# Optimization experiments

Hardware: AMD Instinct MI355X
Metric: run time of the kernel (lower is better)

Reference implementation:

```python
import jax, jax.numpy as jnp
import numpy as np

N_ATOMS = 200_000
AVG_NEIGHBORS = 64
N_PAIRS = N_ATOMS * AVG_NEIGHBORS
BOX = 60.0  # Angstrom, so cutoff=10 masks most random pairs (realistic neighbor-list sparsity)


def setup_inputs() -> dict:
    key = jax.random.key(0)
    kR, ki, kj = jax.random.split(key, 3)
    R = jax.random.uniform(kR, (N_ATOMS, 3), dtype=jnp.float32) * BOX
    idx_i = jax.random.randint(ki, (N_PAIRS,), 0, N_ATOMS, dtype=jnp.int32)
    idx_j = jax.random.randint(kj, (N_PAIRS,), 0, N_ATOMS, dtype=jnp.int32)
    # learned scalar parameters from __init__
    epsilon = jnp.float32(0.238)
    sigma = jnp.float32(3.4)
    cutoff = jnp.float32(10.0)
    return {"R": R, "epsilon": epsilon, "sigma": sigma, "cutoff": cutoff,
            "idx_i": idx_i, "idx_j": idx_j}


def reference(R, epsilon, sigma, cutoff, idx_i, idx_j):
    """LJ 12-6 pairwise potential over a neighbor list.

    Returns (energy [N] per-atom, forces [N,3]).
    Each (i,j) pair appears in both directions in the pair list, hence the 0.5
    factor on per-atom energy; forces accumulate per direction (action-reaction
    handled by the symmetric pair list).
    """
    n_atoms = R.shape[0]
    rij = R[idx_i] - R[idx_j]                     # [P,3] gather
    r2 = jnp.sum(rij * rij, axis=-1)              # [P]
    mask = (r2 < cutoff * cutoff) & (r2 > 1e-10)  # inside cutoff, exclude coincident
    r2s = jnp.where(mask, r2, 1.0)                # safe divide
    sr2 = (sigma * sigma) / r2s
    sr6 = sr2 * sr2 * sr2
    sr12 = sr6 * sr6
    e_pair = jnp.where(mask, 4.0 * epsilon * (sr12 - sr6), 0.0)          # [P]
    f_mag = jnp.where(mask, 24.0 * epsilon * (2.0 * sr12 - sr6) / r2s, 0.0)
    f_pair = f_mag[:, None] * rij                 # [P,3]
    energy = 0.5 * jax.ops.segment_sum(e_pair, idx_i, num_segments=n_atoms)   # [N]
    forces = jax.ops.segment_sum(f_pair, idx_i, num_segments=n_atoms)         # [N,3]
    return energy, forces
```

## Files before the change

### kernel.cpp

```cpp
#include <hip/hip_runtime.h>


typedef int   v4i __attribute__((ext_vector_type(4)));
typedef float v4f __attribute__((ext_vector_type(4)));

#define GRP    8
#define WGT    1024
#define NWG_F  256

__global__ void __launch_bounds__(256) pad_R_kernel(
    const float* __restrict__ R, v4f* __restrict__ Rp, int n_atoms)
{
    int a = blockIdx.x * blockDim.x + threadIdx.x;
    if (a < n_atoms) {
        v4f v;
        v.x = R[3 * a + 0];
        v.y = R[3 * a + 1];
        v.z = R[3 * a + 2];
        v.w = 0.0f;
        Rp[a] = v;
    }
}

__global__ void __launch_bounds__(256) cell_kernel(
    const float* __restrict__ R, const float* __restrict__ cut_p,
    unsigned* __restrict__ packed, int n_atoms)
{
    int t = blockIdx.x * blockDim.x + threadIdx.x;
    int n_thr = (n_atoms + 15) >> 4;
    if (t >= n_thr) return;
    const float inv_cut = 1.0f / cut_p[0];
    int a0 = t << 4;
    unsigned w[3] = {0u, 0u, 0u};
#pragma unroll
    for (int k = 0; k < 16; ++k) {
        int a = a0 + k;
        unsigned c = 0u;
        if (a < n_atoms) {
            int cx = min(7, max(0, (int)(R[3 * a + 0] * inv_cut)));
            int cy = min(7, max(0, (int)(R[3 * a + 1] * inv_cut)));
            c = (unsigned)(cx | (cy << 3));
        }
        int bit = 6 * k, word = bit >> 5, off = bit & 31;
        w[word] |= c << off;
        if (off > 26) w[word + 1] |= c >> (32 - off);
    }
    packed[3 * t + 0] = w[0];
    packed[3 * t + 1] = w[1];
    packed[3 * t + 2] = w[2];
}

__device__ __forceinline__ unsigned cell6(const unsigned char* c8, unsigned a) {
    unsigned bit = a * 6u;
    unsigned by  = bit >> 3;
    unsigned v   = (unsigned)c8[by] | ((unsigned)c8[by + 1] << 8);
    return (v >> (bit & 7u)) & 63u;
}

__device__ __forceinline__ void lj_body(
    v4f A, v4f B, float eps, float s2, float cut2, int gi,
    float* __restrict__ energy, float* __restrict__ forces)
{
    const float dx = A.x - B.x, dy = A.y - B.y, dz = A.z - B.z;
    const float r2 = dx * dx + dy * dy + dz * dz;
    if (r2 < cut2 && r2 > 1e-10f) {
        const float inv  = 1.0f / r2;
        const float sr2  = s2 * inv;
        const float sr6  = sr2 * sr2 * sr2;
        const float sr12 = sr6 * sr6;
        const float e    = 2.0f * eps * (sr12 - sr6);
        const float f    = 24.0f * eps * (2.0f * sr12 - sr6) * inv;
        atomicAdd(&energy[gi], e);
        atomicAdd(&forces[3 * gi + 0], f * dx);
        atomicAdd(&forces[3 * gi + 1], f * dy);
        atomicAdd(&forces[3 * gi + 2], f * dz);
    }
}

__global__ void __launch_bounds__(WGT) lj_fused_kernel(
    const v4f* __restrict__ Rp,
    const unsigned* __restrict__ packed,
    const int* __restrict__ idx_i,
    const int* __restrict__ idx_j,
    const float* __restrict__ eps_p,
    const float* __restrict__ sig_p,
    const float* __restrict__ cut_p,
    float* __restrict__ energy,
    float* __restrict__ forces,
    int n_pairs, int pk_words, int chunk)
{
    extern __shared__ unsigned lds[];
    for (int w = threadIdx.x; w < pk_words; w += WGT)
        lds[w] = packed[w];
    __syncthreads();
    const unsigned char* c8 = (const unsigned char*)lds;

    const float eps  = eps_p[0];
    const float sig  = sig_p[0];
    const float cut  = cut_p[0];
    const float s2   = sig * sig;
    const float cut2 = cut * cut;

    const int cs = blockIdx.x * chunk;
    const int ce = min(cs + chunk, n_pairs);

    for (int p = cs + threadIdx.x * GRP; p < ce; p += WGT * GRP) {
        int is8[GRP], js8[GRP];
        if (p + GRP <= n_pairs) {
            v4i a0 = __builtin_nontemporal_load((const v4i*)idx_i + (p >> 2));
            v4i a1 = __builtin_nontemporal_load((const v4i*)idx_i + (p >> 2) + 1);
            v4i b0 = __builtin_nontemporal_load((const v4i*)idx_j + (p >> 2));
            v4i b1 = __builtin_nontemporal_load((const v4i*)idx_j + (p >> 2) + 1);
            is8[0] = a0.x; is8[1] = a0.y; is8[2] = a0.z; is8[3] = a0.w;
            is8[4] = a1.x; is8[5] = a1.y; is8[6] = a1.z; is8[7] = a1.w;
            js8[0] = b0.x; js8[1] = b0.y; js8[2] = b0.z; js8[3] = b0.w;
            js8[4] = b1.x; js8[5] = b1.y; js8[6] = b1.z; js8[7] = b1.w;
        } else {
#pragma unroll
            for (int k = 0; k < GRP; ++k) {
                bool v = (p + k < n_pairs);
                is8[k] = v ? idx_i[p + k] : 0;
                js8[k] = v ? idx_j[p + k] : 0;
            }
        }

        unsigned m = 0u;
#pragma unroll
        for (int k = 0; k < GRP; ++k) {
            unsigned ci = cell6(c8, (unsigned)is8[k]);
            unsigned cj = cell6(c8, (unsigned)js8[k]);
            int ddx = (int)(ci & 7u) - (int)(cj & 7u);
            int ddy = (int)(ci >> 3) - (int)(cj >> 3);
            bool ok = ((unsigned)(ddx + 1) <= 2u) & ((unsigned)(ddy + 1) <= 2u);
            if (ok) m |= (1u << k);
        }

        v4f Ri[GRP], Rj[GRP];
#pragma unroll
        for (int k = 0; k < GRP; ++k)
            if (m & (1u << k)) { Ri[k] = Rp[is8[k]]; Rj[k] = Rp[js8[k]]; }

#pragma unroll
        for (int k = 0; k < GRP; ++k)
            if (m & (1u << k))
                lj_body(Ri[k], Rj[k], eps, s2, cut2, is8[k], energy, forces);
    }
}

#define PPT 8
__global__ void __launch_bounds__(256) lj_pairs_fb_kernel(
    const v4f* __restrict__ Rp,
    const v4i* __restrict__ idx_i4, const v4i* __restrict__ idx_j4,
    const float* __restrict__ eps_p, const float* __restrict__ sig_p,
    const float* __restrict__ cut_p,
    float* __restrict__ energy, float* __restrict__ forces, int n_oct)
{
    int t = blockIdx.x * blockDim.x + threadIdx.x;
    if (t >= n_oct) return;
    const float eps  = eps_p[0];
    const float sig  = sig_p[0];
    const float cut  = cut_p[0];
    const float s2   = sig * sig;
    const float cut2 = cut * cut;
    v4i ii0 = __builtin_nontemporal_load(idx_i4 + 2 * t);
    v4i ii1 = __builtin_nontemporal_load(idx_i4 + 2 * t + 1);
    v4i jj0 = __builtin_nontemporal_load(idx_j4 + 2 * t);
    v4i jj1 = __builtin_nontemporal_load(idx_j4 + 2 * t + 1);
    int is[PPT] = { ii0.x, ii0.y, ii0.z, ii0.w, ii1.x, ii1.y, ii1.z, ii1.w };
    int js[PPT] = { jj0.x, jj0.y, jj0.z, jj0.w, jj1.x, jj1.y, jj1.z, jj1.w };
    v4f Ri[PPT], Rj[PPT];
#pragma unroll
    for (int k = 0; k < PPT; ++k) Ri[k] = Rp[is[k]];
#pragma unroll
    for (int k = 0; k < PPT; ++k) Rj[k] = Rp[js[k]];
#pragma unroll
    for (int k = 0; k < PPT; ++k)
        lj_body(Ri[k], Rj[k], eps, s2, cut2, is[k], energy, forces);
}

__global__ void lj_pairs_fb_tail_kernel(
    const v4f* __restrict__ Rp,
    const int* __restrict__ idx_i, const int* __restrict__ idx_j,
    const float* __restrict__ eps_p, const float* __restrict__ sig_p,
    const float* __restrict__ cut_p,
    float* __restrict__ energy, float* __restrict__ forces,
    int start, int n_pairs)
{
    int p = start + blockIdx.x * blockDim.x + threadIdx.x;
    if (p >= n_pairs) return;
    const float eps = eps_p[0];
    const float sig = sig_p[0];
    const float cut = cut_p[0];
    lj_body(Rp[idx_i[p]], Rp[idx_j[p]], eps, sig * sig, cut * cut,
            idx_i[p], energy, forces);
}

extern "C" void kernel_launch(void* const* d_in, const int* in_sizes, int n_in,
                              void* d_out, int out_size, void* d_ws, size_t ws_size,
                              hipStream_t stream) {
    const float* R     = (const float*)d_in[0];
    const float* eps_p = (const float*)d_in[1];
    const float* sig_p = (const float*)d_in[2];
    const float* cut_p = (const float*)d_in[3];
    const int*   idx_i = (const int*)d_in[4];
    const int*   idx_j = (const int*)d_in[5];

    const int n_atoms = in_sizes[0] / 3;
    const int n_pairs = in_sizes[4];

    float* energy = (float*)d_out;
    float* forces = (float*)d_out + n_atoms;

    (void)hipMemsetAsync(d_out, 0, (size_t)out_size * sizeof(float), stream);

    char* ws = (char*)d_ws;
    const size_t rp_b     = (((size_t)n_atoms * 16) + 255) & ~(size_t)255;
    const int    n_thr    = (n_atoms + 15) >> 4;
    const int    pk_words = 3 * n_thr + 1;
    const size_t pk_b     = (((size_t)pk_words * 4) + 255) & ~(size_t)255;
    const size_t lds_b    = (((size_t)pk_words * 4) + 15) & ~(size_t)15;

    const bool have_rp    = ws_size >= rp_b;
    const bool use_filter = have_rp && (ws_size >= rp_b + pk_b)
                            && (lds_b <= 160000);

    v4f*      Rp     = (v4f*)ws;
    unsigned* packed = (unsigned*)(ws + rp_b);

    if (have_rp) {
        int blocks = (n_atoms + 255) / 256;
        pad_R_kernel<<<blocks, 256, 0, stream>>>(R, Rp, n_atoms);
    }

    if (use_filter) {
        int cblocks = (n_thr + 255) / 256;
        cell_kernel<<<cblocks, 256, 0, stream>>>(R, cut_p, packed, n_atoms);

        (void)hipFuncSetAttribute((const void*)lj_fused_kernel,
                                  hipFuncAttributeMaxDynamicSharedMemorySize,
                                  (int)lds_b);

        int chunk = (((n_pairs + NWG_F - 1) / NWG_F) + GRP - 1) & ~(GRP - 1);
        lj_fused_kernel<<<NWG_F, WGT, lds_b, stream>>>(
            Rp, packed, idx_i, idx_j, eps_p, sig_p, cut_p,
            energy, forces, n_pairs, pk_words, chunk);
    } else {
        const int n_oct = n_pairs / PPT;
        const int start = n_oct * PPT;
        if (n_oct > 0) {
            int blocks = (n_oct + 255) / 256;
            lj_pairs_fb_kernel<<<blocks, 256, 0, stream>>>(
                Rp, (const v4i*)idx_i, (const v4i*)idx_j,
                eps_p, sig_p, cut_p, energy, forces, n_oct);
        }
        if (start < n_pairs) {
            lj_pairs_fb_tail_kernel<<<1, 64, 0, stream>>>(
                Rp, idx_i, idx_j, eps_p, sig_p, cut_p,
                energy, forces, start, n_pairs);
        }
    }
}
```

Baseline: 192.4 us.

## Fuse prep kernels, use word-aligned cell packing, software-pipeline index loads

```diff
diff --git a/kernel.cpp b/kernel.cpp
--- a/kernel.cpp
+++ b/kernel.cpp
@@ -7,6 +7,33 @@
 #define GRP    8
 #define WGT    1024
 #define NWG_F  256
+
+__global__ void __launch_bounds__(256) prep_kernel(
+    const float* __restrict__ R, const float* __restrict__ cut_p,
+    v4f* __restrict__ Rp, unsigned* __restrict__ packed, int n_atoms)
+{
+    int t = blockIdx.x * blockDim.x + threadIdx.x;
+    int n_grp = (n_atoms + 4) / 5;
+    if (t >= n_grp) return;
+    const float inv_cut = 1.0f / cut_p[0];
+    int a0 = t * 5;
+    unsigned w = 0u;
+#pragma unroll
+    for (int k = 0; k < 5; ++k) {
+        int a = a0 + k;
+        if (a < n_atoms) {
+            float x = R[3 * a + 0];
+            float y = R[3 * a + 1];
+            float z = R[3 * a + 2];
+            v4f v; v.x = x; v.y = y; v.z = z; v.w = 0.0f;
+            Rp[a] = v;
+            int cx = min(7, max(0, (int)(x * inv_cut)));
+            int cy = min(7, max(0, (int)(y * inv_cut)));
+            w |= (unsigned)(cx | (cy << 3)) << (6 * k);
+        }
+    }
+    packed[t] = w;
+}
 
 __global__ void __launch_bounds__(256) pad_R_kernel(
     const float* __restrict__ R, v4f* __restrict__ Rp, int n_atoms)
@@ -22,39 +49,51 @@
     }
 }
 
-__global__ void __launch_bounds__(256) cell_kernel(
-    const float* __restrict__ R, const float* __restrict__ cut_p,
-    unsigned* __restrict__ packed, int n_atoms)
-{
-    int t = blockIdx.x * blockDim.x + threadIdx.x;
-    int n_thr = (n_atoms + 15) >> 4;
-    if (t >= n_thr) return;
-    const float inv_cut = 1.0f / cut_p[0];
-    int a0 = t << 4;
-    unsigned w[3] = {0u, 0u, 0u};
-#pragma unroll
-    for (int k = 0; k < 16; ++k) {
-        int a = a0 + k;
-        unsigned c = 0u;
-        if (a < n_atoms) {
-            int cx = min(7, max(0, (int)(R[3 * a + 0] * inv_cut)));
-            int cy = min(7, max(0, (int)(R[3 * a + 1] * inv_cut)));
-            c = (unsigned)(cx | (cy << 3));
-        }
-        int bit = 6 * k, word = bit >> 5, off = bit & 31;
-        w[word] |= c << off;
-        if (off > 26) w[word + 1] |= c >> (32 - off);
-    }
-    packed[3 * t + 0] = w[0];
-    packed[3 * t + 1] = w[1];
-    packed[3 * t + 2] = w[2];
-}
-
-__device__ __forceinline__ unsigned cell6(const unsigned char* c8, unsigned a) {
-    unsigned bit = a * 6u;
-    unsigned by  = bit >> 3;
-    unsigned v   = (unsigned)c8[by] | ((unsigned)c8[by + 1] << 8);
-    return (v >> (bit & 7u)) & 63u;
+__device__ __forceinline__ unsigned cell6w(const unsigned* __restrict__ lds32,
+                                           unsigned a) {
+    unsigned q = __umulhi(a, 0xCCCCCCCDu) >> 2;
+    unsigned r = a - q * 5u;
+    return (lds32[q] >> (r * 6u)) & 63u;
+}
+
+__device__ __forceinline__ void load_grp(
+    const int* __restrict__ idx_i, const int* __restrict__ idx_j,
+    int p, int n_pairs, int* __restrict__ is8, int* __restrict__ js8)
+{
+    if (p + GRP <= n_pairs) {
+        v4i a0 = __builtin_nontemporal_load((const v4i*)idx_i + (p >> 2));
+        v4i a1 = __builtin_nontemporal_load((const v4i*)idx_i + (p >> 2) + 1);
+        v4i b0 = __builtin_nontemporal_load((const v4i*)idx_j + (p >> 2));
+        v4i b1 = __builtin_nontemporal_load((const v4i*)idx_j + (p >> 2) + 1);
+        is8[0] = a0.x; is8[1] = a0.y; is8[2] = a0.z; is8[3] = a0.w;
+        is8[4] = a1.x; is8[5] = a1.y; is8[6] = a1.z; is8[7] = a1.w;
+        js8[0] = b0.x; js8[1] = b0.y; js8[2] = b0.z; js8[3] = b0.w;
+        js8[4] = b1.x; js8[5] = b1.y; js8[6] = b1.z; js8[7] = b1.w;
+    } else {
+#pragma unroll
+        for (int k = 0; k < GRP; ++k) {
+            bool v = (p + k < n_pairs);
+            is8[k] = v ? idx_i[p + k] : 0;
+            js8[k] = v ? idx_j[p + k] : 0;
+        }
+    }
+}
+
+__device__ __forceinline__ unsigned filt(const unsigned* __restrict__ lds32,
+                                         const int* __restrict__ is8,
+                                         const int* __restrict__ js8)
+{
+    unsigned m = 0u;
+#pragma unroll
+    for (int k = 0; k < GRP; ++k) {
+        unsigned ci = cell6w(lds32, (unsigned)is8[k]);
+        unsigned cj = cell6w(lds32, (unsigned)js8[k]);
+        int ddx = (int)(ci & 7u) - (int)(cj & 7u);
+        int ddy = (int)(ci >> 3) - (int)(cj >> 3);
+        bool ok = ((unsigned)(ddx + 1) <= 2u) & ((unsigned)(ddy + 1) <= 2u);
+        if (ok) m |= (1u << k);
+    }
+    return m;
 }
 
 __device__ __forceinline__ void lj_body(
@@ -93,7 +132,6 @@
     for (int w = threadIdx.x; w < pk_words; w += WGT)
         lds[w] = packed[w];
     __syncthreads();
-    const unsigned char* c8 = (const unsigned char*)lds;
 
     const float eps  = eps_p[0];
     const float sig  = sig_p[0];
@@ -103,47 +141,40 @@
 
     const int cs = blockIdx.x * chunk;
     const int ce = min(cs + chunk, n_pairs);
-
-    for (int p = cs + threadIdx.x * GRP; p < ce; p += WGT * GRP) {
-        int is8[GRP], js8[GRP];
-        if (p + GRP <= n_pairs) {
-            v4i a0 = __builtin_nontemporal_load((const v4i*)idx_i + (p >> 2));
-            v4i a1 = __builtin_nontemporal_load((const v4i*)idx_i + (p >> 2) + 1);
-            v4i b0 = __builtin_nontemporal_load((const v4i*)idx_j + (p >> 2));
-            v4i b1 = __builtin_nontemporal_load((const v4i*)idx_j + (p >> 2) + 1);
-            is8[0] = a0.x; is8[1] = a0.y; is8[2] = a0.z; is8[3] = a0.w;
-            is8[4] = a1.x; is8[5] = a1.y; is8[6] = a1.z; is8[7] = a1.w;
-            js8[0] = b0.x; js8[1] = b0.y; js8[2] = b0.z; js8[3] = b0.w;
-            js8[4] = b1.x; js8[5] = b1.y; js8[6] = b1.z; js8[7] = b1.w;
-        } else {
-#pragma unroll
-            for (int k = 0; k < GRP; ++k) {
-                bool v = (p + k < n_pairs);
-                is8[k] = v ? idx_i[p + k] : 0;
-                js8[k] = v ? idx_j[p + k] : 0;
-            }
-        }
-
-        unsigned m = 0u;
-#pragma unroll
-        for (int k = 0; k < GRP; ++k) {
-            unsigned ci = cell6(c8, (unsigned)is8[k]);
-            unsigned cj = cell6(c8, (unsigned)js8[k]);
-            int ddx = (int)(ci & 7u) - (int)(cj & 7u);
-            int ddy = (int)(ci >> 3) - (int)(cj >> 3);
-            bool ok = ((unsigned)(ddx + 1) <= 2u) & ((unsigned)(ddy + 1) <= 2u);
-            if (ok) m |= (1u << k);
-        }
+    const int STRIDE = WGT * GRP;
+
+    int p0 = cs + (int)threadIdx.x * GRP;
+    if (p0 >= ce) return;
+
+    int isA[GRP], jsA[GRP], isB[GRP], jsB[GRP];
+
+    load_grp(idx_i, idx_j, p0, n_pairs, isA, jsA);
+    unsigned mA = filt(lds, isA, jsA);
+    int p1 = p0 + STRIDE;
+
+    while (true) {
+        const bool h1 = p1 < ce;
+
+        if (h1) load_grp(idx_i, idx_j, p1, n_pairs, isB, jsB);
 
         v4f Ri[GRP], Rj[GRP];
 #pragma unroll
         for (int k = 0; k < GRP; ++k)
-            if (m & (1u << k)) { Ri[k] = Rp[is8[k]]; Rj[k] = Rp[js8[k]]; }
+            if (mA & (1u << k)) { Ri[k] = Rp[isA[k]]; Rj[k] = Rp[jsA[k]]; }
+
+        unsigned mB = 0u;
+        if (h1) mB = filt(lds, isB, jsB);
 
 #pragma unroll
         for (int k = 0; k < GRP; ++k)
-            if (m & (1u << k))
-                lj_body(Ri[k], Rj[k], eps, s2, cut2, is8[k], energy, forces);
+            if (mA & (1u << k))
+                lj_body(Ri[k], Rj[k], eps, s2, cut2, isA[k], energy, forces);
+
+        if (!h1) break;
+#pragma unroll
+        for (int k = 0; k < GRP; ++k) { isA[k] = isB[k]; jsA[k] = jsB[k]; }
+        mA = mB;
+        p1 += STRIDE;
     }
 }
 
@@ -215,8 +246,7 @@
 
     char* ws = (char*)d_ws;
     const size_t rp_b     = (((size_t)n_atoms * 16) + 255) & ~(size_t)255;
-    const int    n_thr    = (n_atoms + 15) >> 4;
-    const int    pk_words = 3 * n_thr + 1;
+    const int    pk_words = (n_atoms + 4) / 5;
     const size_t pk_b     = (((size_t)pk_words * 4) + 255) & ~(size_t)255;
     const size_t lds_b    = (((size_t)pk_words * 4) + 15) & ~(size_t)15;
 
@@ -227,14 +257,9 @@
     v4f*      Rp     = (v4f*)ws;
     unsigned* packed = (unsigned*)(ws + rp_b);
 
-    if (have_rp) {
-        int blocks = (n_atoms + 255) / 256;
-        pad_R_kernel<<<blocks, 256, 0, stream>>>(R, Rp, n_atoms);
-    }
-
     if (use_filter) {
-        int cblocks = (n_thr + 255) / 256;
-        cell_kernel<<<cblocks, 256, 0, stream>>>(R, cut_p, packed, n_atoms);
+        int pblocks = (pk_words + 255) / 256;
+        prep_kernel<<<pblocks, 256, 0, stream>>>(R, cut_p, Rp, packed, n_atoms);
 
         (void)hipFuncSetAttribute((const void*)lj_fused_kernel,
                                   hipFuncAttributeMaxDynamicSharedMemorySize,
@@ -244,12 +269,14 @@
         lj_fused_kernel<<<NWG_F, WGT, lds_b, stream>>>(
             Rp, packed, idx_i, idx_j, eps_p, sig_p, cut_p,
             energy, forces, n_pairs, pk_words, chunk);
-    } else {
+    } else if (have_rp) {
+        int blocks = (n_atoms + 255) / 256;
+        pad_R_kernel<<<blocks, 256, 0, stream>>>(R, Rp, n_atoms);
         const int n_oct = n_pairs / PPT;
         const int start = n_oct * PPT;
         if (n_oct > 0) {
-            int blocks = (n_oct + 255) / 256;
-            lj_pairs_fb_kernel<<<blocks, 256, 0, stream>>>(
+            int fblocks = (n_oct + 255) / 256;
+            lj_pairs_fb_kernel<<<fblocks, 256, 0, stream>>>(
                 Rp, (const v4i*)idx_i, (const v4i*)idx_j,
                 eps_p, sig_p, cut_p, energy, forces, n_oct);
         }
```

Measured after the change: 194.2 us. Within noise of the previous version (+0.9%).
